# Optimization experiments

Measured on AMD Instinct MI355X. Metric: run time of the kernel, lower is better.

The kernel has to match this reference:

```python
import jax, jax.numpy as jnp
import numpy as np

B, DIM, N_SIDE = 32, 256, 32
HEADS, DIM_K, DIM_U = 4, 16, 1
DIM_V = 64  # dim_out // heads
EPS = 1e-5

def _rel_pos_idx(n):
    # matches calc_rel_pos: meshgrid(ij) -> (N,2), pairwise diff + (n-1)
    i = np.arange(n)
    pos = np.stack(np.meshgrid(i, i, indexing='ij'), 0).reshape(2, -1).T  # (N, 2)
    rel = pos[None, :] - pos[:, None] + (n - 1)                            # (N, N, 2)
    return rel[..., 0], rel[..., 1]

def _bn(t, gamma, beta):
    # BatchNorm2d in training mode: batch stats over (B, H, W), biased var
    mu = t.mean(axis=(0, 2, 3), keepdims=True)
    var = t.var(axis=(0, 2, 3), keepdims=True)
    xhat = (t - mu) * jax.lax.rsqrt(var + EPS)
    return xhat * gamma[None, :, None, None] + beta[None, :, None, None]

def setup_inputs() -> dict:
    key = jax.random.key(0)
    ks = jax.random.split(key, 5)
    rl = 2 * N_SIDE - 1
    return {
        'x': jax.random.normal(ks[0], (B, DIM, N_SIDE, N_SIDE), jnp.float32),
        'w_q': jax.random.normal(ks[1], (DIM_K * HEADS, DIM), jnp.float32) * 0.05,
        'w_k': jax.random.normal(ks[2], (DIM_K * DIM_U, DIM), jnp.float32) * 0.05,
        'w_v': jax.random.normal(ks[3], (DIM_V * DIM_U, DIM), jnp.float32) * 0.05,
        'gamma_q': jnp.ones((DIM_K * HEADS,), jnp.float32),
        'beta_q': jnp.zeros((DIM_K * HEADS,), jnp.float32),
        'gamma_v': jnp.ones((DIM_V * DIM_U,), jnp.float32),
        'beta_v': jnp.zeros((DIM_V * DIM_U,), jnp.float32),
        'rel_pos_emb': jax.random.normal(ks[4], (rl, rl, DIM_K, DIM_U), jnp.float32),
    }

def reference(x, w_q, w_k, w_v, gamma_q, beta_q, gamma_v, beta_v, rel_pos_emb):
    b, c, hh, ww = x.shape
    n = hh * ww
    # 1x1 convs as channel contractions
    q = _bn(jnp.einsum('oc,bchw->bohw', w_q, x), gamma_q, beta_q)
    k = jnp.einsum('oc,bchw->bohw', w_k, x)
    v = _bn(jnp.einsum('oc,bchw->bohw', w_v, x), gamma_v, beta_v)
    q = q.reshape(b, HEADS, DIM_K, n)   # b h k n
    k = k.reshape(b, DIM_U, DIM_K, n)   # b u k m
    v = v.reshape(b, DIM_U, DIM_V, n)   # b u v m
    k = jax.nn.softmax(k, axis=-1)
    # content lambda
    lam_c = jnp.einsum('bukm,buvm->bkv', k, v)
    Yc = jnp.einsum('bhkn,bkv->bhvn', q, lam_c)
    # positional lambda via relative-position embedding gather
    ni, mi = _rel_pos_idx(N_SIDE)
    emb = rel_pos_emb[ni, mi]                      # (n, n, k, u)
    lam_p = jnp.einsum('nmku,buvm->bnkv', emb, v)  # dominant compute
    Yp = jnp.einsum('bhkn,bnkv->bhvn', q, lam_p)
    Y = Yc + Yp                                    # b h v n
    return Y.reshape(b, HEADS * DIM_V, hh, ww)
```

## Files before the change

### kernel.cpp

```cpp
#include <hip/hip_runtime.h>

using u16 = unsigned short;
using u32 = unsigned int;

typedef __attribute__((ext_vector_type(4))) float f32x4;
typedef __attribute__((ext_vector_type(4))) u16 u16x4;
typedef __attribute__((ext_vector_type(8))) u16 u16x8;
typedef __attribute__((ext_vector_type(8))) short s16x8;

__device__ __forceinline__ u16 f2bf(float f) {
  u32 x = __builtin_bit_cast(u32, f);
  x += 0x7fffu + ((x >> 16) & 1u);
  return (u16)(x >> 16);
}
__device__ __forceinline__ float bf2f(u16 u) {
  u32 x = ((u32)u) << 16;
  return __builtin_bit_cast(float, x);
}

__device__ __forceinline__ void glds16(const u16* gsrc, u16* ldst) {
  __builtin_amdgcn_global_load_lds(
      (const __attribute__((address_space(1))) unsigned int*)gsrc,
      (__attribute__((address_space(3))) unsigned int*)ldst, 16, 0, 0);
}

__global__ __launch_bounds__(256) void k_prep(
    const float* __restrict__ wq, const float* __restrict__ wk,
    const float* __restrict__ wv, const float* __restrict__ R,
    u16* __restrict__ Wb, u16* __restrict__ APre)
{
  const int blk = blockIdx.x;
  const int t = threadIdx.x;
  if (blk < 144) {
    const int o = blk;
    const float* src = (o < 64) ? (wq + o * 256)
                     : (o < 80) ? (wk + (o - 64) * 256)
                                : (wv + (o - 80) * 256);
    Wb[o * 256 + t] = f2bf(src[t]);
  } else {
    const int di = blk - 144;
    const int w = t >> 6, l = t & 63;
    const int g = l >> 4, k = l & 15;
    for (int j1 = w; j1 < 32; j1 += 4) {
      u16x8 o8;
#pragma unroll
      for (int e = 0; e < 8; ++e) {
        int dj = 8 * g + e - j1 + 31;
        o8[e] = f2bf(R[(di * 63 + dj) * 16 + k]);
      }
      *(u16x8*)(APre + ((di * 32 + j1) * 64 + l) * 8) = o8;
    }
  }
}

union ProjSmem {
  u16 XLb[64][264];
  float SS[2][160];
};

__global__ __launch_bounds__(256) void k_proj(
    const float* __restrict__ x, const u16* __restrict__ Wb,
    float* __restrict__ q_raw, float* __restrict__ k_raw,
    float* __restrict__ v_raw,
    float* __restrict__ qs1, float* __restrict__ qs2,
    float* __restrict__ vs1, float* __restrict__ vs2)
{
  __shared__ ProjSmem PS;
  const int b  = blockIdx.x >> 4;
  const int p0 = (blockIdx.x & 15) * 64;
  const int t  = threadIdx.x;

  {
    const int p4 = (t & 15) * 4;
    const int cb = (t >> 4);
#pragma unroll
    for (int i = 0; i < 8; ++i) {
      const int c = 2 * (i * 16 + cb);
      f32x4 xa = *(const f32x4*)&x[(b * 256 + c) * 1024 + p0 + p4];
      f32x4 xb = *(const f32x4*)&x[(b * 256 + c + 1) * 1024 + p0 + p4];
#pragma unroll
      for (int j = 0; j < 4; ++j) {
        u32 pk = (u32)f2bf(xa[j]) | ((u32)f2bf(xb[j]) << 16);
        *(u32*)&PS.XLb[p4 + j][c] = pk;
      }
    }
  }
  __syncthreads();

  const int w  = t >> 6;
  const int l  = t & 63;
  const int g  = l >> 4;
  const int cc = l & 15;
  const int p  = p0 + w * 16 + cc;

  f32x4 acc[9];
  const f32x4 fz = {0.f, 0.f, 0.f, 0.f};
#pragma unroll
  for (int mt = 0; mt < 9; ++mt) acc[mt] = fz;

#pragma unroll
  for (int ko = 0; ko < 8; ++ko) {
    s16x8 bfr = *(const s16x8*)&PS.XLb[w * 16 + cc][ko * 32 + g * 8];
#pragma unroll
    for (int mt = 0; mt < 9; ++mt) {
      s16x8 afr = *(const s16x8*)&Wb[(mt * 16 + cc) * 256 + ko * 32 + g * 8];
      acc[mt] = __builtin_amdgcn_mfma_f32_16x16x32_bf16(afr, bfr, acc[mt], 0, 0, 0);
    }
  }

#pragma unroll
  for (int mt = 0; mt < 9; ++mt) {
#pragma unroll
    for (int r = 0; r < 4; ++r) {
      const int o = mt * 16 + 4 * g + r;
      const float val = acc[mt][r];
      if (mt < 4)       q_raw[(b * 64 + o) * 1024 + p] = val;
      else if (mt == 4) k_raw[(b * 16 + (o - 64)) * 1024 + p] = val;
      else              v_raw[(b * 64 + (o - 80)) * 1024 + p] = val;
    }
  }

  __syncthreads();
  {
    float* ss = &PS.SS[0][0];
    for (int i = t; i < 320; i += 256) ss[i] = 0.f;
  }
  __syncthreads();
#pragma unroll
  for (int mt = 0; mt < 9; ++mt) {
    if (mt == 4) continue;
#pragma unroll
    for (int r = 0; r < 4; ++r) {
      float s1 = acc[mt][r];
      float s2 = s1 * s1;
#pragma unroll
      for (int off = 1; off < 16; off <<= 1) {
        s1 += __shfl_xor(s1, off);
        s2 += __shfl_xor(s2, off);
      }
      if (cc == 0) {
        const int o = mt * 16 + 4 * g + r;
        atomicAdd(&PS.SS[0][o], s1);
        atomicAdd(&PS.SS[1][o], s2);
      }
    }
  }
  __syncthreads();
  if (t < 64) {
    atomicAdd(&qs1[t], PS.SS[0][t]);
    atomicAdd(&qs2[t], PS.SS[1][t]);
  } else if (t >= 80 && t < 144) {
    atomicAdd(&vs1[t - 80], PS.SS[0][t]);
    atomicAdd(&vs2[t - 80], PS.SS[1][t]);
  }
}

__global__ __launch_bounds__(256) void k_soft(
    const float* __restrict__ k_raw,
    float* __restrict__ kmax, float* __restrict__ kinv)
{
  const int t = threadIdx.x;
  const int w = t >> 6, lane = t & 63;
  const int row = blockIdx.x * 4 + w;
  const f32x4* kr4 = (const f32x4*)(k_raw + row * 1024 + lane * 16);
  f32x4 a0 = kr4[0], a1 = kr4[1], a2 = kr4[2], a3 = kr4[3];
  float mx = -3.0e38f;
#pragma unroll
  for (int j = 0; j < 4; ++j)
    mx = fmaxf(mx, fmaxf(fmaxf(a0[j], a1[j]), fmaxf(a2[j], a3[j])));
#pragma unroll
  for (int off = 32; off; off >>= 1) mx = fmaxf(mx, __shfl_xor(mx, off));
  float s = 0.f;
#pragma unroll
  for (int j = 0; j < 4; ++j)
    s += __expf(a0[j] - mx) + __expf(a1[j] - mx)
       + __expf(a2[j] - mx) + __expf(a3[j] - mx);
#pragma unroll
  for (int off = 32; off; off >>= 1) s += __shfl_xor(s, off);
  if (lane == 0) { kmax[row] = mx; kinv[row] = 1.0f / s; }
}

__global__ __launch_bounds__(256) void k_nl(
    const float* __restrict__ v_raw,
    const float* __restrict__ vs1, const float* __restrict__ vs2,
    const float* __restrict__ gv, const float* __restrict__ bv,
    const float* __restrict__ k_raw, const float* __restrict__ kmax,
    const float* __restrict__ kinv,
    u16* __restrict__ vnF, float* __restrict__ lam_c)
{
  __shared__ float VN[64][136];
  __shared__ float KE[16][132];
  const int b  = blockIdx.x >> 3;
  const int m0 = (blockIdx.x & 7) * 128;
  const int t  = threadIdx.x;
  {
    const int v = t & 63, mseg = t >> 6;
    const float invN = 1.0f / 32768.0f;
    const float mu = vs1[v] * invN;
    const float var = vs2[v] * invN - mu * mu;
    const float sc = rsqrtf(var + 1e-5f) * gv[v];
    const float bi = bv[v] - mu * sc;
    const int i2 = (m0 >> 5) + mseg;
    const float* src = v_raw + (b * 64 + v) * 1024 + i2 * 32;
    u16* dstF = vnF + ((b * 32 + i2) * 4 + (v >> 4)) * 512 + (v & 15) * 8;
#pragma unroll
    for (int lg = 0; lg < 4; ++lg) {
      f32x4 a = *(const f32x4*)(src + lg * 8);
      f32x4 c = *(const f32x4*)(src + lg * 8 + 4);
      f32x4 na, nc;
      u16x8 o8;
#pragma unroll
      for (int j = 0; j < 4; ++j) {
        na[j] = a[j] * sc + bi;
        nc[j] = c[j] * sc + bi;
        o8[j] = f2bf(na[j]);
        o8[4 + j] = f2bf(nc[j]);
      }
      *(f32x4*)&VN[v][mseg * 32 + lg * 8] = na;
      *(f32x4*)&VN[v][mseg * 32 + lg * 8 + 4] = nc;
      *(u16x8*)(dstF + lg * 128) = o8;
    }
  }
  {
    const int kc = t >> 4, mm = (t & 15) * 8;
    const int row = b * 16 + kc;
    const float* kr = k_raw + row * 1024 + m0 + mm;
    const float mx = kmax[row], iv = kinv[row];
#pragma unroll
    for (int j = 0; j < 8; ++j) KE[kc][mm + j] = __expf(kr[j] - mx) * iv;
  }
  __syncthreads();
  const int kc = t & 15, vg = t >> 4;
  float acc[4] = {0.f, 0.f, 0.f, 0.f};
  for (int m4 = 0; m4 < 128; m4 += 4) {
    f32x4 ke = *(const f32x4*)&KE[kc][m4];
#pragma unroll
    for (int j = 0; j < 4; ++j) {
      f32x4 vv = *(const f32x4*)&VN[vg * 4 + j][m4];
      acc[j] += ke[0] * vv[0] + ke[1] * vv[1] + ke[2] * vv[2] + ke[3] * vv[3];
    }
  }
#pragma unroll
  for (int j = 0; j < 4; ++j)
    atomicAdd(&lam_c[(b * 16 + kc) * 64 + vg * 4 + j], acc[j]);
}

__device__ __forceinline__ void load_a4(s16x8 (&dst)[4], const u16* ab)
{
#pragma unroll
  for (int j = 0; j < 4; ++j) dst[j] = *(const s16x8*)(ab + j * 512);
}

union KMainSmem {
  u16 BB[2][8192];
  float YL[256][18];
};

__global__ __launch_bounds__(256, 4) void k_main(
    const u16* __restrict__ APre, const u16* __restrict__ vnF,
    const float* __restrict__ q_raw, const float* __restrict__ lam_c,
    const float* __restrict__ qs1, const float* __restrict__ qs2,
    const float* __restrict__ gq, const float* __restrict__ bq,
    float* __restrict__ out)
{
  __shared__ alignas(16) KMainSmem S;
  __shared__ float QL[64][17];
  const int bid  = blockIdx.x;
  const int xcd  = bid & 7;
  const int sb   = bid >> 3;
  const int b    = xcd * 4 + (sb & 3);
  const int rest = sb >> 2;
  const int i1   = rest >> 1;
  const int half = rest & 1;
  const int t  = threadIdx.x;
  const int w  = t >> 6;
  const int l  = t & 63;
  const int g  = l >> 4;
  const int c  = l & 15;
  const int j1base = half * 16 + w * 4;

  const u16* vF = vnF + b * 65536;

  f32x4 acc[4][4];
  const f32x4 fz = {0.f, 0.f, 0.f, 0.f};
#pragma unroll
  for (int nn = 0; nn < 4; ++nn)
#pragma unroll
    for (int tt = 0; tt < 4; ++tt) acc[nn][tt] = fz;

  {
    const int o = t >> 2, ns = (t & 3) * 4;
    const float invN = 1.0f / 32768.0f;
    const float mu = qs1[o] * invN;
    const float var = qs2[o] * invN - mu * mu;
    const float rs = rsqrtf(var + 1e-5f);
    const float sc = rs * gq[o];
    const float bi = bq[o] - mu * sc;
    f32x4 qa = *(const f32x4*)&q_raw[(b * 64 + o) * 1024 + i1 * 32 + half * 16 + ns];
#pragma unroll
    for (int j = 0; j < 4; ++j) QL[o][ns + j] = qa[j] * sc + bi;
  }
  {
    const u16* src = vF + w * 2048 + l * 8;
    u16* dst = &S.BB[0][w * 2048];
#pragma unroll
    for (int j = 0; j < 4; ++j) glds16(src + j * 512, dst + j * 512);
  }

  s16x8 afrP[4], afrQ[4];
  const u16* aBase = APre + ((31 - i1) * 32 + j1base) * 512 + l * 8;
  load_a4(afrP, aBase);
  __syncthreads();

  for (int p = 0; p < 8; ++p) {
    const int cur = p & 1;
    const bool pf = (p < 7);
    if (pf) {
      const u16* src = vF + (p + 1) * 8192 + w * 2048 + l * 8;
      u16* dst = &S.BB[cur ^ 1][w * 2048];
#pragma unroll
      for (int j = 0; j < 4; ++j) glds16(src + j * 512, dst + j * 512);
    }
    __builtin_amdgcn_sched_barrier(0);
    const u16* ap = aBase + 4 * p * 16384;
    s16x8 bfr[4];
#pragma unroll
    for (int s = 0; s < 4; ++s) {
#pragma unroll
      for (int tt = 0; tt < 4; ++tt)
        bfr[tt] = *(const s16x8*)&S.BB[cur][s * 2048 + tt * 512 + l * 8];
      if (s < 3) {
        if (s & 1) load_a4(afrP, ap + (s + 1) * 16384);
        else       load_a4(afrQ, ap + (s + 1) * 16384);
      } else if (pf) {
        load_a4(afrP, ap + 4 * 16384);
      }
      const s16x8* A = (s & 1) ? afrQ : afrP;
#pragma unroll
      for (int nn = 0; nn < 4; ++nn)
#pragma unroll
        for (int tt = 0; tt < 4; ++tt)
          acc[nn][tt] = __builtin_amdgcn_mfma_f32_16x16x32_bf16(
              A[nn], bfr[tt], acc[nn][tt], 0, 0, 0);
    }
    asm volatile("s_waitcnt vmcnt(4)" ::: "memory");
    __builtin_amdgcn_sched_barrier(0);
    __builtin_amdgcn_s_barrier();
    __builtin_amdgcn_sched_barrier(0);
  }

  {
    const float* lcb = lam_c + b * 1024;
#pragma unroll
    for (int tt = 0; tt < 4; ++tt)
#pragma unroll
      for (int r = 0; r < 4; ++r) {
        const float lv = lcb[(4 * g + r) * 64 + tt * 16 + c];
#pragma unroll
        for (int nn = 0; nn < 4; ++nn) acc[nn][tt][r] += lv;
      }
  }
#pragma unroll
  for (int nn = 0; nn < 4; ++nn) {
    const int j1loc = w * 4 + nn;
#pragma unroll
    for (int h = 0; h < 4; ++h) {
      const float q0 = QL[h * 16 + 4 * g + 0][j1loc];
      const float q1 = QL[h * 16 + 4 * g + 1][j1loc];
      const float q2 = QL[h * 16 + 4 * g + 2][j1loc];
      const float q3 = QL[h * 16 + 4 * g + 3][j1loc];
#pragma unroll
      for (int tt = 0; tt < 4; ++tt) {
        float sY = q0 * acc[nn][tt][0] + q1 * acc[nn][tt][1]
                 + q2 * acc[nn][tt][2] + q3 * acc[nn][tt][3];
        sY += __shfl_xor(sY, 16);
        sY += __shfl_xor(sY, 32);
        if (g == h) S.YL[h * 64 + tt * 16 + c][j1loc] = sY;
      }
    }
  }
  __syncthreads();
#pragma unroll
  for (int it = 0; it < 4; ++it) {
    const int o  = (t >> 2) + it * 64;
    const int nf = (t & 3) * 4;
    f32x4 v4 = *(const f32x4*)&S.YL[o][nf];
    *(f32x4*)&out[(b * 256 + o) * 1024 + i1 * 32 + half * 16 + nf] = v4;
  }
}

extern "C" void kernel_launch(void* const* d_in, const int* in_sizes, int n_in,
                              void* d_out, int out_size, void* d_ws, size_t ws_size,
                              hipStream_t stream) {
  const float* x  = (const float*)d_in[0];
  const float* wq = (const float*)d_in[1];
  const float* wk = (const float*)d_in[2];
  const float* wv = (const float*)d_in[3];
  const float* gq = (const float*)d_in[4];
  const float* bq = (const float*)d_in[5];
  const float* gv = (const float*)d_in[6];
  const float* bv = (const float*)d_in[7];
  const float* R  = (const float*)d_in[8];
  float* out = (float*)d_out;

  float* wsf   = (float*)d_ws;
  float* q_raw = wsf;
  float* k_raw = q_raw + 32 * 64 * 1024;
  float* v_raw = k_raw + 32 * 16 * 1024;
  float* lam_c = v_raw + 32 * 64 * 1024;
  float* qs1   = lam_c + 32 * 16 * 64;
  float* qs2   = qs1 + 64;
  float* vs1   = qs2 + 64;
  float* vs2   = vs1 + 64;
  float* kmax  = vs2 + 64;
  float* kinv  = kmax + 512;
  u16*   vn    = (u16*)(kinv + 512);
  u16*   vnF   = vn + 32 * 64 * 1024;
  u16*   APre  = vnF + 32 * 65536;
  u16*   Wb    = APre + 63 * 32 * 512;

  hipMemsetAsync(lam_c, 0, (32 * 16 * 64 + 256) * sizeof(float), stream);
  k_prep<<<207, 256, 0, stream>>>(wq, wk, wv, R, Wb, APre);
  k_proj<<<512, 256, 0, stream>>>(x, Wb, q_raw, k_raw, v_raw, qs1, qs2, vs1, vs2);
  k_soft<<<128, 256, 0, stream>>>(k_raw, kmax, kinv);
  k_nl<<<256, 256, 0, stream>>>(v_raw, vs1, vs2, gv, bv, k_raw, kmax, kinv, vnF, lam_c);
  k_main<<<2048, 256, 0, stream>>>(APre, vnF, q_raw, lam_c, qs1, qs2, gq, bq, out);
}
```

Baseline: 138.3 us.

## Share staged A tiles in LDS across two batches per 512-thread block

```diff
diff --git a/kernel.cpp b/kernel.cpp
--- a/kernel.cpp
+++ b/kernel.cpp
@@ -245,18 +245,15 @@
     atomicAdd(&lam_c[(b * 16 + kc) * 64 + vg * 4 + j], acc[j]);
 }
 
-__device__ __forceinline__ void load_a4(s16x8 (&dst)[4], const u16* ab)
-{
-#pragma unroll
-  for (int j = 0; j < 4; ++j) dst[j] = *(const s16x8*)(ab + j * 512);
-}
-
 union KMainSmem {
-  u16 BB[2][8192];
-  float YL[256][18];
+  struct {
+    u16 AL[2][8192];
+    u16 BL[2][2][2048];
+  } st;
+  float YL[2][256][18];
 };
 
-__global__ __launch_bounds__(256, 4) void k_main(
+__global__ __launch_bounds__(512, 4) void k_main(
     const u16* __restrict__ APre, const u16* __restrict__ vnF,
     const float* __restrict__ q_raw, const float* __restrict__ lam_c,
     const float* __restrict__ qs1, const float* __restrict__ qs2,
@@ -264,22 +261,25 @@
     float* __restrict__ out)
 {
   __shared__ alignas(16) KMainSmem S;
-  __shared__ float QL[64][17];
+  __shared__ float QL[2][64][17];
   const int bid  = blockIdx.x;
   const int xcd  = bid & 7;
   const int sb   = bid >> 3;
-  const int b    = xcd * 4 + (sb & 3);
-  const int rest = sb >> 2;
+  const int pl   = sb & 1;
+  const int rest = sb >> 1;
   const int i1   = rest >> 1;
   const int half = rest & 1;
+  const int bBase = xcd * 4 + pl * 2;
   const int t  = threadIdx.x;
   const int w  = t >> 6;
+  const int bw = w >> 2;
+  const int wl = w & 3;
   const int l  = t & 63;
   const int g  = l >> 4;
   const int c  = l & 15;
-  const int j1base = half * 16 + w * 4;
-
-  const u16* vF = vnF + b * 65536;
+  const int b  = bBase + bw;
+
+  const u16* vFw = vnF + b * 65536;
 
   f32x4 acc[4][4];
   const f32x4 fz = {0.f, 0.f, 0.f, 0.f};
@@ -288,62 +288,50 @@
 #pragma unroll
     for (int tt = 0; tt < 4; ++tt) acc[nn][tt] = fz;
 
-  {
-    const int o = t >> 2, ns = (t & 3) * 4;
+  auto stage = [&](int p, int nb) {
+    const u16* asrc = APre + ((p - i1 + 31) * 32 + half * 16) * 512
+                    + w * 1024 + l * 8;
+    glds16(asrc, &S.st.AL[nb][w * 1024]);
+    glds16(asrc + 512, &S.st.AL[nb][w * 1024 + 512]);
+    const u16* bsrc = vFw + p * 2048 + wl * 512 + l * 8;
+    glds16(bsrc, &S.st.BL[nb][bw][wl * 512]);
+  };
+
+  stage(0, 0);
+  {
+    const int bw2 = t >> 8;
+    const int o = (t & 255) >> 2, ns = (t & 3) * 4;
     const float invN = 1.0f / 32768.0f;
     const float mu = qs1[o] * invN;
     const float var = qs2[o] * invN - mu * mu;
     const float rs = rsqrtf(var + 1e-5f);
     const float sc = rs * gq[o];
     const float bi = bq[o] - mu * sc;
-    f32x4 qa = *(const f32x4*)&q_raw[(b * 64 + o) * 1024 + i1 * 32 + half * 16 + ns];
-#pragma unroll
-    for (int j = 0; j < 4; ++j) QL[o][ns + j] = qa[j] * sc + bi;
-  }
-  {
-    const u16* src = vF + w * 2048 + l * 8;
-    u16* dst = &S.BB[0][w * 2048];
-#pragma unroll
-    for (int j = 0; j < 4; ++j) glds16(src + j * 512, dst + j * 512);
-  }
-
-  s16x8 afrP[4], afrQ[4];
-  const u16* aBase = APre + ((31 - i1) * 32 + j1base) * 512 + l * 8;
-  load_a4(afrP, aBase);
-  __syncthreads();
-
-  for (int p = 0; p < 8; ++p) {
+    f32x4 qa = *(const f32x4*)&q_raw[((bBase + bw2) * 64 + o) * 1024
+                                     + i1 * 32 + half * 16 + ns];
+#pragma unroll
+    for (int j = 0; j < 4; ++j) QL[bw2][o][ns + j] = qa[j] * sc + bi;
+  }
+  __syncthreads();
+
+  for (int p = 0; p < 32; ++p) {
     const int cur = p & 1;
-    const bool pf = (p < 7);
-    if (pf) {
-      const u16* src = vF + (p + 1) * 8192 + w * 2048 + l * 8;
-      u16* dst = &S.BB[cur ^ 1][w * 2048];
-#pragma unroll
-      for (int j = 0; j < 4; ++j) glds16(src + j * 512, dst + j * 512);
-    }
+    if (p < 31) stage(p + 1, cur ^ 1);
     __builtin_amdgcn_sched_barrier(0);
-    const u16* ap = aBase + 4 * p * 16384;
-    s16x8 bfr[4];
-#pragma unroll
-    for (int s = 0; s < 4; ++s) {
+    s16x8 afr[4], bfr[4];
+#pragma unroll
+    for (int nn = 0; nn < 4; ++nn)
+      afr[nn] = *(const s16x8*)&S.st.AL[cur][(wl * 4 + nn) * 512 + l * 8];
+#pragma unroll
+    for (int tt = 0; tt < 4; ++tt)
+      bfr[tt] = *(const s16x8*)&S.st.BL[cur][bw][tt * 512 + l * 8];
+#pragma unroll
+    for (int nn = 0; nn < 4; ++nn)
 #pragma unroll
       for (int tt = 0; tt < 4; ++tt)
-        bfr[tt] = *(const s16x8*)&S.BB[cur][s * 2048 + tt * 512 + l * 8];
-      if (s < 3) {
-        if (s & 1) load_a4(afrP, ap + (s + 1) * 16384);
-        else       load_a4(afrQ, ap + (s + 1) * 16384);
-      } else if (pf) {
-        load_a4(afrP, ap + 4 * 16384);
-      }
-      const s16x8* A = (s & 1) ? afrQ : afrP;
-#pragma unroll
-      for (int nn = 0; nn < 4; ++nn)
-#pragma unroll
-        for (int tt = 0; tt < 4; ++tt)
-          acc[nn][tt] = __builtin_amdgcn_mfma_f32_16x16x32_bf16(
-              A[nn], bfr[tt], acc[nn][tt], 0, 0, 0);
-    }
-    asm volatile("s_waitcnt vmcnt(4)" ::: "memory");
+        acc[nn][tt] = __builtin_amdgcn_mfma_f32_16x16x32_bf16(
+            afr[nn], bfr[tt], acc[nn][tt], 0, 0, 0);
+    asm volatile("s_waitcnt vmcnt(0)" ::: "memory");
     __builtin_amdgcn_sched_barrier(0);
     __builtin_amdgcn_s_barrier();
     __builtin_amdgcn_sched_barrier(0);
@@ -362,30 +350,31 @@
   }
 #pragma unroll
   for (int nn = 0; nn < 4; ++nn) {
-    const int j1loc = w * 4 + nn;
+    const int j1loc = wl * 4 + nn;
 #pragma unroll
     for (int h = 0; h < 4; ++h) {
-      const float q0 = QL[h * 16 + 4 * g + 0][j1loc];
-      const float q1 = QL[h * 16 + 4 * g + 1][j1loc];
-      const float q2 = QL[h * 16 + 4 * g + 2][j1loc];
-      const float q3 = QL[h * 16 + 4 * g + 3][j1loc];
+      const float q0 = QL[bw][h * 16 + 4 * g + 0][j1loc];
+      const float q1 = QL[bw][h * 16 + 4 * g + 1][j1loc];
+      const float q2 = QL[bw][h * 16 + 4 * g + 2][j1loc];
+      const float q3 = QL[bw][h * 16 + 4 * g + 3][j1loc];
 #pragma unroll
       for (int tt = 0; tt < 4; ++tt) {
         float sY = q0 * acc[nn][tt][0] + q1 * acc[nn][tt][1]
                  + q2 * acc[nn][tt][2] + q3 * acc[nn][tt][3];
         sY += __shfl_xor(sY, 16);
         sY += __shfl_xor(sY, 32);
-        if (g == h) S.YL[h * 64 + tt * 16 + c][j1loc] = sY;
+        if (g == h) S.YL[bw][h * 64 + tt * 16 + c][j1loc] = sY;
       }
     }
   }
   __syncthreads();
 #pragma unroll
   for (int it = 0; it < 4; ++it) {
-    const int o  = (t >> 2) + it * 64;
+    const int bw2 = t >> 8;
+    const int o  = ((t & 255) >> 2) + it * 64;
     const int nf = (t & 3) * 4;
-    f32x4 v4 = *(const f32x4*)&S.YL[o][nf];
-    *(f32x4*)&out[(b * 256 + o) * 1024 + i1 * 32 + half * 16 + nf] = v4;
+    f32x4 v4 = *(const f32x4*)&S.YL[bw2][o][nf];
+    *(f32x4*)&out[((bBase + bw2) * 256 + o) * 1024 + i1 * 32 + half * 16 + nf] = v4;
   }
 }
 
@@ -424,5 +413,5 @@
   k_proj<<<512, 256, 0, stream>>>(x, Wb, q_raw, k_raw, v_raw, qs1, qs2, vs1, vs2);
   k_soft<<<128, 256, 0, stream>>>(k_raw, kmax, kinv);
   k_nl<<<256, 256, 0, stream>>>(v_raw, vs1, vs2, gv, bv, k_raw, kmax, kinv, vnF, lam_c);
-  k_main<<<2048, 256, 0, stream>>>(APre, vnF, q_raw, lam_c, qs1, qs2, gq, bq, out);
-}
+  k_main<<<1024, 512, 0, stream>>>(APre, vnF, q_raw, lam_c, qs1, qs2, gq, bq, out);
+}
```

Result: slower. 141.1 us (+2.0%).

## Deepen k_main pipeline to triple-buffered LDS and two-ahead A-fragment prefetch

Applied to the files above, without the earlier changes.

```diff
diff --git a/kernel.cpp b/kernel.cpp
--- a/kernel.cpp
+++ b/kernel.cpp
@@ -252,11 +252,11 @@
 }
 
 union KMainSmem {
-  u16 BB[2][8192];
+  u16 BB[3][8192];
   float YL[256][18];
 };
 
-__global__ __launch_bounds__(256, 4) void k_main(
+__global__ __launch_bounds__(256, 3) void k_main(
     const u16* __restrict__ APre, const u16* __restrict__ vnF,
     const float* __restrict__ q_raw, const float* __restrict__ lam_c,
     const float* __restrict__ qs1, const float* __restrict__ qs2,
@@ -288,6 +288,15 @@
 #pragma unroll
     for (int tt = 0; tt < 4; ++tt) acc[nn][tt] = fz;
 
+  auto stage = [&](int ph) {
+    const u16* src = vF + ph * 8192 + w * 2048 + l * 8;
+    u16* dst = &S.BB[ph % 3][w * 2048];
+#pragma unroll
+    for (int j = 0; j < 4; ++j) glds16(src + j * 512, dst + j * 512);
+  };
+
+  stage(0);
+  stage(1);
   {
     const int o = t >> 2, ns = (t & 3) * 4;
     const float invN = 1.0f / 32768.0f;
@@ -300,50 +309,42 @@
 #pragma unroll
     for (int j = 0; j < 4; ++j) QL[o][ns + j] = qa[j] * sc + bi;
   }
-  {
-    const u16* src = vF + w * 2048 + l * 8;
-    u16* dst = &S.BB[0][w * 2048];
-#pragma unroll
-    for (int j = 0; j < 4; ++j) glds16(src + j * 512, dst + j * 512);
-  }
-
-  s16x8 afrP[4], afrQ[4];
+  s16x8 A0[4], A1[4], A2[4], A3[4];
   const u16* aBase = APre + ((31 - i1) * 32 + j1base) * 512 + l * 8;
-  load_a4(afrP, aBase);
+  load_a4(A0, aBase);
+  load_a4(A1, aBase + 16384);
   __syncthreads();
 
   for (int p = 0; p < 8; ++p) {
-    const int cur = p & 1;
-    const bool pf = (p < 7);
-    if (pf) {
-      const u16* src = vF + (p + 1) * 8192 + w * 2048 + l * 8;
-      u16* dst = &S.BB[cur ^ 1][w * 2048];
-#pragma unroll
-      for (int j = 0; j < 4; ++j) glds16(src + j * 512, dst + j * 512);
-    }
+    const int cur = p % 3;
+    if (p < 6) stage(p + 2);
     __builtin_amdgcn_sched_barrier(0);
     const u16* ap = aBase + 4 * p * 16384;
-    s16x8 bfr[4];
-#pragma unroll
-    for (int s = 0; s < 4; ++s) {
-#pragma unroll
-      for (int tt = 0; tt < 4; ++tt)
-        bfr[tt] = *(const s16x8*)&S.BB[cur][s * 2048 + tt * 512 + l * 8];
-      if (s < 3) {
-        if (s & 1) load_a4(afrP, ap + (s + 1) * 16384);
-        else       load_a4(afrQ, ap + (s + 1) * 16384);
-      } else if (pf) {
-        load_a4(afrP, ap + 4 * 16384);
-      }
-      const s16x8* A = (s & 1) ? afrQ : afrP;
-#pragma unroll
-      for (int nn = 0; nn < 4; ++nn)
-#pragma unroll
-        for (int tt = 0; tt < 4; ++tt)
-          acc[nn][tt] = __builtin_amdgcn_mfma_f32_16x16x32_bf16(
-              A[nn], bfr[tt], acc[nn][tt], 0, 0, 0);
-    }
-    asm volatile("s_waitcnt vmcnt(4)" ::: "memory");
+
+#define SUBBODY(s, Acur, Anext)                                               \
+    {                                                                         \
+      s16x8 bfr[4];                                                           \
+      _Pragma("unroll")                                                       \
+      for (int tt = 0; tt < 4; ++tt)                                          \
+        bfr[tt] = *(const s16x8*)&S.BB[cur][(s) * 2048 + tt * 512 + l * 8];   \
+      if (4 * p + (s) + 2 < 32)                                               \
+        load_a4(Anext, ap + ((s) + 2) * 16384);                               \
+      __builtin_amdgcn_s_setprio(1);                                          \
+      _Pragma("unroll")                                                       \
+      for (int nn = 0; nn < 4; ++nn)                                          \
+        _Pragma("unroll")                                                     \
+        for (int tt = 0; tt < 4; ++tt)                                        \
+          acc[nn][tt] = __builtin_amdgcn_mfma_f32_16x16x32_bf16(              \
+              Acur[nn], bfr[tt], acc[nn][tt], 0, 0, 0);                       \
+      __builtin_amdgcn_s_setprio(0);                                          \
+    }
+
+    SUBBODY(0, A0, A2)
+    SUBBODY(1, A1, A3)
+    SUBBODY(2, A2, A0)
+    SUBBODY(3, A3, A1)
+#undef SUBBODY
+
     __builtin_amdgcn_sched_barrier(0);
     __builtin_amdgcn_s_barrier();
     __builtin_amdgcn_sched_barrier(0);
```

Result: no change. 138.8 us (+0.4%).

## Load B fragments directly from global into registers, drop LDS double buffer

Applied to the files above, without the earlier changes.

```diff
diff --git a/kernel.cpp b/kernel.cpp
--- a/kernel.cpp
+++ b/kernel.cpp
@@ -16,12 +16,6 @@
 __device__ __forceinline__ float bf2f(u16 u) {
   u32 x = ((u32)u) << 16;
   return __builtin_bit_cast(float, x);
-}
-
-__device__ __forceinline__ void glds16(const u16* gsrc, u16* ldst) {
-  __builtin_amdgcn_global_load_lds(
-      (const __attribute__((address_space(1))) unsigned int*)gsrc,
-      (__attribute__((address_space(3))) unsigned int*)ldst, 16, 0, 0);
 }
 
 __global__ __launch_bounds__(256) void k_prep(
@@ -245,26 +239,21 @@
     atomicAdd(&lam_c[(b * 16 + kc) * 64 + vg * 4 + j], acc[j]);
 }
 
-__device__ __forceinline__ void load_a4(s16x8 (&dst)[4], const u16* ab)
-{
-#pragma unroll
-  for (int j = 0; j < 4; ++j) dst[j] = *(const s16x8*)(ab + j * 512);
-}
-
-union KMainSmem {
-  u16 BB[2][8192];
-  float YL[256][18];
-};
-
-__global__ __launch_bounds__(256, 4) void k_main(
+__device__ __forceinline__ void load4(s16x8 (&dst)[4], const u16* p)
+{
+#pragma unroll
+  for (int j = 0; j < 4; ++j) dst[j] = *(const s16x8*)(p + j * 512);
+}
+
+__global__ __launch_bounds__(256, 3) void k_main(
     const u16* __restrict__ APre, const u16* __restrict__ vnF,
     const float* __restrict__ q_raw, const float* __restrict__ lam_c,
     const float* __restrict__ qs1, const float* __restrict__ qs2,
     const float* __restrict__ gq, const float* __restrict__ bq,
     float* __restrict__ out)
 {
-  __shared__ alignas(16) KMainSmem S;
   __shared__ float QL[64][17];
+  __shared__ float YL[256][18];
   const int bid  = blockIdx.x;
   const int xcd  = bid & 7;
   const int sb   = bid >> 3;
@@ -279,7 +268,8 @@
   const int c  = l & 15;
   const int j1base = half * 16 + w * 4;
 
-  const u16* vF = vnF + b * 65536;
+  const u16* aBase = APre + ((31 - i1) * 32 + j1base) * 512 + l * 8;
+  const u16* bBase = vnF + b * 65536 + l * 8;
 
   f32x4 acc[4][4];
   const f32x4 fz = {0.f, 0.f, 0.f, 0.f};
@@ -300,54 +290,31 @@
 #pragma unroll
     for (int j = 0; j < 4; ++j) QL[o][ns + j] = qa[j] * sc + bi;
   }
-  {
-    const u16* src = vF + w * 2048 + l * 8;
-    u16* dst = &S.BB[0][w * 2048];
-#pragma unroll
-    for (int j = 0; j < 4; ++j) glds16(src + j * 512, dst + j * 512);
-  }
-
-  s16x8 afrP[4], afrQ[4];
-  const u16* aBase = APre + ((31 - i1) * 32 + j1base) * 512 + l * 8;
-  load_a4(afrP, aBase);
-  __syncthreads();
-
-  for (int p = 0; p < 8; ++p) {
-    const int cur = p & 1;
-    const bool pf = (p < 7);
-    if (pf) {
-      const u16* src = vF + (p + 1) * 8192 + w * 2048 + l * 8;
-      u16* dst = &S.BB[cur ^ 1][w * 2048];
-#pragma unroll
-      for (int j = 0; j < 4; ++j) glds16(src + j * 512, dst + j * 512);
-    }
-    __builtin_amdgcn_sched_barrier(0);
-    const u16* ap = aBase + 4 * p * 16384;
-    s16x8 bfr[4];
-#pragma unroll
-    for (int s = 0; s < 4; ++s) {
+
+  s16x8 Aa[4], Ba[4], Ab[4], Bb[4];
+  load4(Aa, aBase);
+  load4(Ba, bBase);
+  for (int it = 0; it < 16; ++it) {
+    load4(Ab, aBase + (2 * it + 1) * 16384);
+    load4(Bb, bBase + (2 * it + 1) * 2048);
+#pragma unroll
+    for (int nn = 0; nn < 4; ++nn)
 #pragma unroll
       for (int tt = 0; tt < 4; ++tt)
-        bfr[tt] = *(const s16x8*)&S.BB[cur][s * 2048 + tt * 512 + l * 8];
-      if (s < 3) {
-        if (s & 1) load_a4(afrP, ap + (s + 1) * 16384);
-        else       load_a4(afrQ, ap + (s + 1) * 16384);
-      } else if (pf) {
-        load_a4(afrP, ap + 4 * 16384);
-      }
-      const s16x8* A = (s & 1) ? afrQ : afrP;
-#pragma unroll
-      for (int nn = 0; nn < 4; ++nn)
-#pragma unroll
-        for (int tt = 0; tt < 4; ++tt)
-          acc[nn][tt] = __builtin_amdgcn_mfma_f32_16x16x32_bf16(
-              A[nn], bfr[tt], acc[nn][tt], 0, 0, 0);
-    }
-    asm volatile("s_waitcnt vmcnt(4)" ::: "memory");
-    __builtin_amdgcn_sched_barrier(0);
-    __builtin_amdgcn_s_barrier();
-    __builtin_amdgcn_sched_barrier(0);
-  }
+        acc[nn][tt] = __builtin_amdgcn_mfma_f32_16x16x32_bf16(
+            Aa[nn], Ba[tt], acc[nn][tt], 0, 0, 0);
+    if (it < 15) {
+      load4(Aa, aBase + (2 * it + 2) * 16384);
+      load4(Ba, bBase + (2 * it + 2) * 2048);
+    }
+#pragma unroll
+    for (int nn = 0; nn < 4; ++nn)
+#pragma unroll
+      for (int tt = 0; tt < 4; ++tt)
+        acc[nn][tt] = __builtin_amdgcn_mfma_f32_16x16x32_bf16(
+            Ab[nn], Bb[tt], acc[nn][tt], 0, 0, 0);
+  }
+  __syncthreads();
 
   {
     const float* lcb = lam_c + b * 1024;
@@ -375,7 +342,7 @@
                  + q2 * acc[nn][tt][2] + q3 * acc[nn][tt][3];
         sY += __shfl_xor(sY, 16);
         sY += __shfl_xor(sY, 32);
-        if (g == h) S.YL[h * 64 + tt * 16 + c][j1loc] = sY;
+        if (g == h) YL[h * 64 + tt * 16 + c][j1loc] = sY;
       }
     }
   }
@@ -384,7 +351,7 @@
   for (int it = 0; it < 4; ++it) {
     const int o  = (t >> 2) + it * 64;
     const int nf = (t & 3) * 4;
-    f32x4 v4 = *(const f32x4*)&S.YL[o][nf];
+    f32x4 v4 = *(const f32x4*)&YL[o][nf];
     *(f32x4*)&out[(b * 256 + o) * 1024 + i1 * 32 + half * 16 + nf] = v4;
   }
 }
```

Result: slower. 156.5 us (+13.2%).
